# Optimization experiments

Measured on AMD Instinct MI355X. Metric: run time of the kernel, lower is better.

## Reference

```python
import jax, jax.numpy as jnp
import numpy as np
from jax import lax

B, CIN, H, W = 32, 256, 28, 28
COUT, KS, KEXP = 256, 3, 4
HIDDEN = int(CIN * 0.25)  # ratio hard-coded to 0.25 in the module


def setup_inputs() -> dict:
    key = jax.random.key(0)
    k1, k2, k3, k4 = jax.random.split(key, 4)
    x = jax.random.normal(k1, (B, CIN, H, W), dtype=jnp.float32)
    # SE (InvertedEx) params: fc1 (1x1 conv, no bias), fc2 (1x1 conv, bias)
    fc1_w = jax.random.normal(k2, (HIDDEN, CIN), dtype=jnp.float32) * np.float32(np.sqrt(2.0 / CIN))
    fc2_w = jax.random.normal(k3, (KEXP * COUT, HIDDEN), dtype=jnp.float32) * np.float32(np.sqrt(2.0 / HIDDEN))
    fc2_b = jnp.zeros((KEXP * COUT,), dtype=jnp.float32)
    # K expert conv kernels, he_std = sqrt(2) * (CIN*KS^2)^-0.5
    he_std = np.float32(np.sqrt(2.0) * (CIN * KS * KS) ** -0.5)
    weight = jax.random.normal(k4, (KEXP, COUT, CIN, KS, KS), dtype=jnp.float32) * he_std
    return {"x": x, "fc1_w": fc1_w, "fc2_w": fc2_w, "fc2_b": fc2_b, "weight": weight}


def reference(x, fc1_w, fc2_w, fc2_b, weight):
    # --- SE routing ---
    pooled = jnp.mean(x, axis=(2, 3))                        # [B, CIN]
    h = jax.nn.relu(pooled @ fc1_w.T)                        # [B, HIDDEN]
    y = (h @ fc2_w.T + fc2_b).reshape(B, KEXP, COUT)         # [B, K, COUT]
    prob = jax.nn.softmax(y / jnp.sqrt(jnp.float32(HIDDEN)), axis=1)  # softmax over K
    # --- aggregate per-sample kernels ---
    agg_w = jnp.einsum('bko,koihw->boihw', prob, weight)     # [B, COUT, CIN, KS, KS]
    # --- per-sample conv (batched implicit GEMM via vmap) ---
    def conv1(xi, wi):
        return lax.conv_general_dilated(
            xi[None], wi, window_strides=(1, 1), padding=((1, 1), (1, 1)),
            dimension_numbers=('NCHW', 'OIHW', 'NCHW'))[0]
    out = jax.vmap(conv1)(x, agg_w)                          # [B, COUT, H, W]
    return out
```

## Files before the change

### kernel.cpp

```cpp
#include <hip/hip_runtime.h>
#include <math.h>

#define B_    32
#define CIN_  256
#define HW_   784
#define H_    28
#define W_    28
#define COUT_ 256
#define KEXP_ 4
#define HID_  64

typedef short short8 __attribute__((ext_vector_type(8)));
typedef unsigned short ushort4v __attribute__((ext_vector_type(4)));
typedef unsigned short ushort8v __attribute__((ext_vector_type(8)));
typedef float floatx16 __attribute__((ext_vector_type(16)));

#define AS1 __attribute__((address_space(1)))
#define AS3 __attribute__((address_space(3)))
__device__ __forceinline__ void glds16(const void* g, void* l) {
    __builtin_amdgcn_global_load_lds((const AS1 unsigned int*)g,
                                     (AS3 unsigned int*)l, 16, 0, 0);
}
#define VMW(N) asm volatile("s_waitcnt vmcnt(" #N ")" ::: "memory")
#define SB()   __builtin_amdgcn_sched_barrier(0)

__device__ __forceinline__ unsigned short f2bf(float f) {
    union { float f; unsigned int u; } v; v.f = f;
    unsigned int r = (v.u + 0x7FFFu + ((v.u >> 16) & 1u)) >> 16;
    return (unsigned short)r;
}

__global__ __launch_bounds__(256) void xpose_pool_kernel(const float* __restrict__ x,
                                                         unsigned short* __restrict__ x_t,
                                                         float* __restrict__ partial,
                                                         float* __restrict__ zp) {
    __shared__ float tile[32][33];
    int bid = blockIdx.x;
    int b   = bid / 200;
    int rem = bid - b * 200;
    int icg = rem / 25;
    int pxt = rem % 25;
    int ic0 = icg * 32;
    int px0 = pxt * 32;
    int t = threadIdx.x;
    if (bid == 0 && t == 0) {
        float4 z; z.x = 0.f; z.y = 0.f; z.z = 0.f; z.w = 0.f;
        *(float4*)zp = z;
    }
    int c = t & 31, rr = t >> 5;
    #pragma unroll
    for (int r = 0; r < 4; ++r) {
        int icr = rr + r * 8;
        int px = px0 + c;
        float v = (px < HW_) ? x[((size_t)(b * CIN_ + ic0 + icr)) * HW_ + px] : 0.f;
        tile[icr][c] = v;
    }
    __syncthreads();
    #pragma unroll
    for (int r = 0; r < 4; ++r) {
        int pxr = rr + r * 8;
        int px = px0 + pxr;
        if (px < HW_)
            x_t[((size_t)b * HW_ + px) * CIN_ + ic0 + c] = f2bf(tile[c][pxr]);
    }
    if (t < 32) {
        float s = 0.f;
        #pragma unroll
        for (int cc = 0; cc < 32; ++cc) s += tile[t][cc];
        partial[((size_t)b * 25 + pxt) * CIN_ + ic0 + t] = s * (1.0f / HW_);
    }
}

__global__ __launch_bounds__(256) void pool_kernel(const float* __restrict__ x,
                                                   float* __restrict__ pooled) {
    int w = blockIdx.x * 4 + (threadIdx.x >> 6);
    int lane = threadIdx.x & 63;
    const float* p = x + (size_t)w * HW_;
    float s = 0.f;
    for (int i = lane; i < HW_; i += 64) s += p[i];
    for (int off = 32; off; off >>= 1) s += __shfl_down(s, off);
    if (lane == 0) pooled[w] = s * (1.0f / HW_);
}

__global__ __launch_bounds__(256) void se3_kernel(const float* __restrict__ partial,
                                                  const float* __restrict__ fc1_w,
                                                  const float* __restrict__ fc2_w,
                                                  const float* __restrict__ fc2_b,
                                                  float* __restrict__ prob) {
    __shared__ float pl[CIN_];
    __shared__ float h[HID_];
    __shared__ float wb[16640];
    int b = blockIdx.x, t = threadIdx.x;
    {
        float s = 0.f;
        for (int pt = 0; pt < 25; ++pt)
            s += partial[((size_t)b * 25 + pt) * CIN_ + t];
        pl[t] = s;
    }
    #pragma unroll
    for (int i = 0; i < 16; ++i) {
        int l = t + i * 256;
        float4 v = *(const float4*)(fc1_w + (size_t)l * 4);
        int r = l >> 6, cc = (l & 63) * 4;
        float* dst = &wb[r * 257 + cc];
        dst[0] = v.x; dst[1] = v.y; dst[2] = v.z; dst[3] = v.w;
    }
    __syncthreads();
    if (t < HID_) {
        float s = 0.f;
        const float* wr = &wb[t * 257];
        for (int c = 0; c < CIN_; ++c) s += pl[c] * wr[c];
        h[t] = fmaxf(s, 0.f);
    }
    float yk[KEXP_];
    for (int k = 0; k < KEXP_; ++k) {
        __syncthreads();
        #pragma unroll
        for (int i = 0; i < 16; ++i) {
            int l = t + i * 256;
            float4 v = *(const float4*)(fc2_w + (size_t)k * COUT_ * HID_ + (size_t)l * 4);
            int o = l >> 4, jj = (l & 15) * 4;
            float* dst = &wb[o * 65 + jj];
            dst[0] = v.x; dst[1] = v.y; dst[2] = v.z; dst[3] = v.w;
        }
        __syncthreads();
        float s = fc2_b[k * COUT_ + t];
        const float* wr = &wb[t * 65];
        #pragma unroll
        for (int j = 0; j < HID_; ++j) s += h[j] * wr[j];
        yk[k] = s * 0.125f;
    }
    float m = yk[0];
    for (int k = 1; k < KEXP_; ++k) m = fmaxf(m, yk[k]);
    float e[KEXP_], sum = 0.f;
    for (int k = 0; k < KEXP_; ++k) { e[k] = expf(yk[k] - m); sum += e[k]; }
    float inv = 1.0f / sum;
    for (int k = 0; k < KEXP_; ++k)
        prob[b * (KEXP_ * COUT_) + k * COUT_ + t] = e[k] * inv;
}

__global__ __launch_bounds__(256) void se2_kernel(const float* __restrict__ pooled,
                                                  const float* __restrict__ fc1_w,
                                                  const float* __restrict__ fc2_w,
                                                  const float* __restrict__ fc2_b,
                                                  float* __restrict__ prob) {
    __shared__ float pl[CIN_];
    __shared__ float h[HID_];
    __shared__ float wb[16640];
    int b = blockIdx.x, t = threadIdx.x;
    pl[t] = pooled[b * CIN_ + t];
    #pragma unroll
    for (int i = 0; i < 16; ++i) {
        int l = t + i * 256;
        float4 v = *(const float4*)(fc1_w + (size_t)l * 4);
        int r = l >> 6, cc = (l & 63) * 4;
        float* dst = &wb[r * 257 + cc];
        dst[0] = v.x; dst[1] = v.y; dst[2] = v.z; dst[3] = v.w;
    }
    __syncthreads();
    if (t < HID_) {
        float s = 0.f;
        const float* wr = &wb[t * 257];
        for (int c = 0; c < CIN_; ++c) s += pl[c] * wr[c];
        h[t] = fmaxf(s, 0.f);
    }
    float yk[KEXP_];
    for (int k = 0; k < KEXP_; ++k) {
        __syncthreads();
        #pragma unroll
        for (int i = 0; i < 16; ++i) {
            int l = t + i * 256;
            float4 v = *(const float4*)(fc2_w + (size_t)k * COUT_ * HID_ + (size_t)l * 4);
            int o = l >> 4, jj = (l & 15) * 4;
            float* dst = &wb[o * 65 + jj];
            dst[0] = v.x; dst[1] = v.y; dst[2] = v.z; dst[3] = v.w;
        }
        __syncthreads();
        float s = fc2_b[k * COUT_ + t];
        const float* wr = &wb[t * 65];
        #pragma unroll
        for (int j = 0; j < HID_; ++j) s += h[j] * wr[j];
        yk[k] = s * 0.125f;
    }
    float m = yk[0];
    for (int k = 1; k < KEXP_; ++k) m = fmaxf(m, yk[k]);
    float e[KEXP_], sum = 0.f;
    for (int k = 0; k < KEXP_; ++k) { e[k] = expf(yk[k] - m); sum += e[k]; }
    float inv = 1.0f / sum;
    for (int k = 0; k < KEXP_; ++k)
        prob[b * (KEXP_ * COUT_) + k * COUT_ + t] = e[k] * inv;
}

__global__ __launch_bounds__(256) void agg4_kernel(const float* __restrict__ weight,
                                                   const float* __restrict__ prob,
                                                   unsigned short* __restrict__ agg) {
    __shared__ float wlds[4][32][145];
    int gid = blockIdx.x;
    int og  = gid & 7;
    int icc = (gid >> 3) & 3;
    int kk  = (gid >> 5) & 3;
    int bh  = gid >> 7;
    int oc0 = og * 32;
    int ic0 = icc * 64 + kk * 16;
    int t = threadIdx.x;

    #pragma unroll
    for (int i = 0; i < 18; ++i) {
        int idx = t + i * 256;
        int k  = idx / 1152;
        int r  = idx - k * 1152;
        int oc = r / 36;
        int f4 = r - oc * 36;
        float4 v = *(const float4*)(weight + ((size_t)(k * COUT_ + oc0 + oc) * CIN_ + ic0) * 9 + f4 * 4);
        float* dst = &wlds[k][oc][f4 * 4];
        dst[0] = v.x; dst[1] = v.y; dst[2] = v.z; dst[3] = v.w;
    }

    int lane = t & 63, wv = t >> 6;
    int ml = lane & 31, kh = lane >> 5;

    float pbr[4][4];
    #pragma unroll
    for (int bi = 0; bi < 4; ++bi) {
        int b = bh * 16 + wv * 4 + bi;
        #pragma unroll
        for (int k = 0; k < 4; ++k)
            pbr[bi][k] = prob[(size_t)b * (KEXP_ * COUT_) + k * COUT_ + oc0 + ml];
    }
    __syncthreads();

    for (int rs = 0; rs < 9; ++rs) {
        float wreg[4][8];
        #pragma unroll
        for (int k = 0; k < 4; ++k)
            #pragma unroll
            for (int j = 0; j < 8; ++j)
                wreg[k][j] = wlds[k][ml][(kh * 8 + j) * 9 + rs];
        #pragma unroll
        for (int bi = 0; bi < 4; ++bi) {
            int b = bh * 16 + wv * 4 + bi;
            ushort8v pack;
            #pragma unroll
            for (int j = 0; j < 8; ++j) {
                float s = pbr[bi][0] * wreg[0][j] + pbr[bi][1] * wreg[1][j]
                        + pbr[bi][2] * wreg[2][j] + pbr[bi][3] * wreg[3][j];
                pack[j] = f2bf(s);
            }
            *(ushort8v*)(agg + (size_t)(b * 16 + icc * 4 + kk) * 36864
                             + (size_t)rs * 4096 + og * 512 + lane * 8) = pack;
        }
    }
}

__global__ __launch_bounds__(256, 2) void conv_mfma8_kernel(const unsigned short* __restrict__ x_t,
                                                            const unsigned short* __restrict__ agg,
                                                            const float* __restrict__ zp,
                                                            float* __restrict__ out) {
    __shared__ __align__(16) short Xs[2][6720];
    __shared__ __align__(16) short Alds[24576];

    int gid = blockIdx.x;
    int b      = gid & 31;
    int half   = (gid >> 5) & 1;
    int oc0    = half * 128;
    int rowblk = gid >> 6;
    int py0 = rowblk * 4;

    int t = threadIdx.x;
    int lane = t & 63, w = t >> 6;
    int ml = lane & 31, kh = lane >> 5;
    int og = half * 4 + w;
    int kh16 = kh << 4;

    floatx16 acc[4];
    #pragma unroll
    for (int j = 0; j < 4; ++j)
        #pragma unroll
        for (int r = 0; r < 16; ++r) acc[j][r] = 0.f;

    const unsigned short* xtb = x_t + (size_t)b * HW_ * CIN_;
    const unsigned short* ag  = agg + (size_t)b * 589824 + og * 512 + lane * 8;

    int off[3][6];
    #pragma unroll
    for (int dx = 0; dx < 3; ++dx)
        #pragma unroll
        for (int r = 0; r < 6; ++r) {
            int a = ml + dx + 35 * r;
            off[dx][r] = a * 64 + ((((a & 3) ^ ((a >> 2) & 1))) << 4);
        }

    auto stageXs = [&](int cc, int bb) {
        #pragma unroll
        for (int i = 0; i < 3; ++i) {
            int l = t + i * 256;
            int pos = l >> 2, gl = l & 3;
            int g8 = gl ^ (pos & 3) ^ ((pos >> 2) & 1);
            int row = pos / 35, col = pos - row * 35;
            int gy = py0 - 1 + row, gx = col - 1;
            const void* src = ((unsigned)gy < 28u && (unsigned)gx < 28u)
                ? (const void*)(xtb + ((size_t)(gy * W_ + gx)) * CIN_ + cc * 32 + g8 * 8)
                : (const void*)zp;
            glds16(src, &Xs[bb][(w * 64 + i * 256) * 8]);
        }
        if (w < 2) {
            int l = t + 768;
            int pos = l >> 2, gl = l & 3;
            int g8 = gl ^ (pos & 3) ^ ((pos >> 2) & 1);
            int row = pos / 35, col = pos - row * 35;
            int gy = py0 - 1 + row, gx = col - 1;
            const void* src = (l < 840 && (unsigned)gy < 28u && (unsigned)gx < 28u)
                ? (const void*)(xtb + ((size_t)(gy * W_ + gx)) * CIN_ + cc * 32 + g8 * 8)
                : (const void*)zp;
            if (l < 840)
                glds16(src, &Xs[bb][(w * 64 + 768) * 8]);
        }
    };

    auto dmaA = [&](int gg) {
        int c3  = gg / 6;
        int icc = c3 >> 1;
        int kk4 = (c3 & 1) * 2 + (gg % 6) / 3;
        int dx3 = gg % 3;
        const unsigned short* sp = ag + icc * 147456 + kk4 * 36864 + dx3 * 4096;
        short* d = &Alds[((w * 4 + (gg & 3)) * 3) * 512];
        glds16(sp,         d);
        glds16(sp + 12288, d + 512);
        glds16(sp + 24576, d + 1024);
    };

    stageXs(0, 0);  SB();
    dmaA(0);        SB();
    dmaA(1);        SB();
    dmaA(2);        SB();
    VMW(6);         SB();
    __builtin_amdgcn_s_barrier();

    short8 Areg[2][3];
    #pragma unroll
    for (int tap = 0; tap < 3; ++tap)
        Areg[0][tap] = *(const short8*)&Alds[((w * 4 + 0) * 3 + tap) * 512 + lane * 8];

    #pragma unroll
    for (int g = 0; g < 48; ++g) {
        const int c  = g / 6;
        const int s  = g % 6;
        const int kk = s / 3;
        const int dx = g % 3;

        if (g + 3 < 48)      { dmaA(g + 3);                  SB(); }
        if (s == 3 && c < 7) { stageXs(c + 1, (c + 1) & 1);  SB(); }

        if (g == 45)      { VMW(3); }
        else if (g == 46) { VMW(0); }
        else if (g < 45 && s >= 3 && c < 7) { VMW(9); }
        else if (g < 47)  { VMW(6); }
        SB();

        if (g < 47) {
            #pragma unroll
            for (int tap = 0; tap < 3; ++tap)
                Areg[(g + 1) & 1][tap] =
                    *(const short8*)&Alds[((w * 4 + ((g + 1) & 3)) * 3 + tap) * 512 + lane * 8];
        }

        const char* xbc = (const char*)&Xs[c & 1][0];
        const int kxor = (kk << 5) | kh16;
        #pragma unroll
        for (int r = 0; r < 6; ++r) {
            short8 Bf = *(const short8*)(xbc + (off[dx][r] ^ kxor));
            if (r <= 3)
                acc[r]     = __builtin_amdgcn_mfma_f32_32x32x16_bf16(Areg[g & 1][0], Bf, acc[r], 0, 0, 0);
            if (r >= 1 && r <= 4)
                acc[r - 1] = __builtin_amdgcn_mfma_f32_32x32x16_bf16(Areg[g & 1][1], Bf, acc[r - 1], 0, 0, 0);
            if (r >= 2)
                acc[r - 2] = __builtin_amdgcn_mfma_f32_32x32x16_bf16(Areg[g & 1][2], Bf, acc[r - 2], 0, 0, 0);
        }

        if (s == 5 && c < 7) {
            VMW(6);  SB();
            __builtin_amdgcn_s_barrier();
        }
    }

    if (ml < W_) {
        #pragma unroll
        for (int j = 0; j < 4; ++j) {
            float* op = out + ((size_t)(b * COUT_ + oc0 + w * 32)) * HW_ + (py0 + j) * W_ + ml;
            #pragma unroll
            for (int r = 0; r < 16; ++r) {
                int ocd = (r & 3) + 8 * (r >> 2) + 4 * kh;
                op[(size_t)ocd * HW_] = acc[j][r];
            }
        }
    }
}

__global__ __launch_bounds__(256) void conv_kernel(const float* __restrict__ x,
                                                   const float* __restrict__ weight,
                                                   const float* __restrict__ prob,
                                                   float* __restrict__ out) {
    __shared__ float xs[30 * 30];
    __shared__ float wagg[8][32][12];
    __shared__ float pl[KEXP_][8];

    int b  = blockIdx.x >> 5;
    int o0 = (blockIdx.x & 31) * 8;
    int t  = threadIdx.x;

    if (t < 32) {
        int k = t >> 3, oc = t & 7;
        pl[k][oc] = prob[b * (KEXP_ * COUT_) + k * COUT_ + o0 + oc];
    }
    int p0 = t;
    int pr[4], pc[4];
    bool pv[4];
    #pragma unroll
    for (int j = 0; j < 4; ++j) {
        int p = p0 + j * 256;
        pv[j] = p < HW_;
        pr[j] = p / W_;
        pc[j] = p % W_;
    }
    float acc[8][4];
    #pragma unroll
    for (int oc = 0; oc < 8; ++oc)
        #pragma unroll
        for (int j = 0; j < 4; ++j) acc[oc][j] = 0.f;

    int aoc = t >> 5, aii = t & 31;

    for (int ic0 = 0; ic0 < CIN_; ic0 += 32) {
        __syncthreads();
        {
            float w9[9];
            #pragma unroll
            for (int j = 0; j < 9; ++j) w9[j] = 0.f;
            int i = ic0 + aii;
            #pragma unroll
            for (int k = 0; k < KEXP_; ++k) {
                float pk = pl[k][aoc];
                const float* wp = weight + ((size_t)(k * COUT_ + o0 + aoc) * CIN_ + i) * 9;
                #pragma unroll
                for (int j = 0; j < 9; ++j) w9[j] += pk * wp[j];
            }
            #pragma unroll
            for (int j = 0; j < 9; ++j) wagg[aoc][aii][j] = w9[j];
        }
        for (int ii = 0; ii < 32; ++ii) {
            int i = ic0 + ii;
            __syncthreads();
            const float* xp = x + (size_t)(b * CIN_ + i) * HW_;
            for (int e = t; e < 900; e += 256) {
                int ry = e / 30, cx = e - ry * 30;
                int gy = ry - 1, gx = cx - 1;
                float v = 0.f;
                if ((unsigned)gy < 28u && (unsigned)gx < 28u) v = xp[gy * W_ + gx];
                xs[e] = v;
            }
            __syncthreads();
            float xv[4][9];
            #pragma unroll
            for (int j = 0; j < 4; ++j) {
                if (pv[j]) {
                    const float* xr = &xs[pr[j] * 30 + pc[j]];
                    xv[j][0] = xr[0];  xv[j][1] = xr[1];  xv[j][2] = xr[2];
                    xv[j][3] = xr[30]; xv[j][4] = xr[31]; xv[j][5] = xr[32];
                    xv[j][6] = xr[60]; xv[j][7] = xr[61]; xv[j][8] = xr[62];
                } else {
                    #pragma unroll
                    for (int q = 0; q < 9; ++q) xv[j][q] = 0.f;
                }
            }
            #pragma unroll
            for (int oc = 0; oc < 8; ++oc) {
                float4 wa = *(const float4*)&wagg[oc][ii][0];
                float4 wb2 = *(const float4*)&wagg[oc][ii][4];
                float  wc = wagg[oc][ii][8];
                #pragma unroll
                for (int j = 0; j < 4; ++j) {
                    acc[oc][j] += xv[j][0] * wa.x + xv[j][1] * wa.y + xv[j][2] * wa.z
                                + xv[j][3] * wa.w + xv[j][4] * wb2.x + xv[j][5] * wb2.y
                                + xv[j][6] * wb2.z + xv[j][7] * wb2.w + xv[j][8] * wc;
                }
            }
        }
    }
    #pragma unroll
    for (int oc = 0; oc < 8; ++oc) {
        float* op = out + (size_t)(b * COUT_ + o0 + oc) * HW_ + p0;
        #pragma unroll
        for (int j = 0; j < 4; ++j)
            if (pv[j]) op[j * 256] = acc[oc][j];
    }
}

extern "C" void kernel_launch(void* const* d_in, const int* in_sizes, int n_in,
                              void* d_out, int out_size, void* d_ws, size_t ws_size,
                              hipStream_t stream) {
    const float* x     = (const float*)d_in[0];
    const float* fc1_w = (const float*)d_in[1];
    const float* fc2_w = (const float*)d_in[2];
    const float* fc2_b = (const float*)d_in[3];
    const float* weight= (const float*)d_in[4];
    float* out = (float*)d_out;

    char* ws = (char*)d_ws;
    float* prob = (float*)(ws);
    unsigned short* x_t = (unsigned short*)(ws + 131072);
    unsigned short* agg = (unsigned short*)(ws + 12976128);
    float* partial = (float*)(ws + 12976128);
    float* zp   = (float*)(ws + 50724864);
    const size_t WS_NEED = 50724864 + 4096;

    if (ws_size >= WS_NEED) {
        xpose_pool_kernel<<<B_ * 8 * 25, 256, 0, stream>>>(x, x_t, partial, zp);
        se3_kernel<<<B_, 256, 0, stream>>>(partial, fc1_w, fc2_w, fc2_b, prob);
        agg4_kernel<<<256, 256, 0, stream>>>(weight, prob, agg);
        conv_mfma8_kernel<<<448, 256, 0, stream>>>(x_t, agg, zp, out);
    } else {
        float* pooled = (float*)(ws + 131072);
        pool_kernel<<<(B_ * CIN_) / 4, 256, 0, stream>>>(x, pooled);
        se2_kernel<<<B_, 256, 0, stream>>>(pooled, fc1_w, fc2_w, fc2_b, prob);
        conv_kernel<<<B_ * (COUT_ / 8), 256, 0, stream>>>(x, weight, prob, out);
    }
}
```

Measured before the change: 145.3 us.

## Enlarge conv tile to seven output rows per block with new LDS swizzle

The implicit-GEMM conv kernel now computes 7 output rows per block instead of 4, so the grid shrinks from 448 to 256 blocks and each A (aggregated weight) fragment is reused across more MFMAs. The X staging buffer grows for the taller halo and gets a new pair-based XOR swizzle. The A prefetch ring drops from 4 to 3 slots with a restructured per-chunk loop and a peeled final chunk. The goal is to cut weight reloads and per-block overhead. The cost is 7 accumulators per thread, so more register pressure, and 256 blocks may not fill all CUs on the GPU.

New measurement: 148.6 us. 1.02x slower.

```diff
diff --git a/kernel.cpp b/kernel.cpp
--- a/kernel.cpp
+++ b/kernel.cpp
@@ -252,140 +252,146 @@
     }
 }
 
-__global__ __launch_bounds__(256, 2) void conv_mfma8_kernel(const unsigned short* __restrict__ x_t,
+__global__ __launch_bounds__(256, 2) void conv_mfma9_kernel(const unsigned short* __restrict__ x_t,
                                                             const unsigned short* __restrict__ agg,
                                                             const float* __restrict__ zp,
                                                             float* __restrict__ out) {
-    __shared__ __align__(16) short Xs[2][6720];
-    __shared__ __align__(16) short Alds[24576];
+    __shared__ __align__(16) short Xs[2][10080];
+    __shared__ __align__(16) short Alds[18432];
 
     int gid = blockIdx.x;
     int b      = gid & 31;
     int half   = (gid >> 5) & 1;
     int oc0    = half * 128;
     int rowblk = gid >> 6;
-    int py0 = rowblk * 4;
+    int py0 = rowblk * 7;
 
     int t = threadIdx.x;
     int lane = t & 63, w = t >> 6;
     int ml = lane & 31, kh = lane >> 5;
     int og = half * 4 + w;
-    int kh16 = kh << 4;
-
-    floatx16 acc[4];
-    #pragma unroll
-    for (int j = 0; j < 4; ++j)
+
+    floatx16 acc[7];
+    #pragma unroll
+    for (int j = 0; j < 7; ++j)
         #pragma unroll
         for (int r = 0; r < 16; ++r) acc[j][r] = 0.f;
 
     const unsigned short* xtb = x_t + (size_t)b * HW_ * CIN_;
     const unsigned short* ag  = agg + (size_t)b * 589824 + og * 512 + lane * 8;
 
-    int off[3][6];
+    int off0[3][9];
     #pragma unroll
     for (int dx = 0; dx < 3; ++dx)
         #pragma unroll
-        for (int r = 0; r < 6; ++r) {
+        for (int r = 0; r < 9; ++r) {
             int a = ml + dx + 35 * r;
-            off[dx][r] = a * 64 + ((((a & 3) ^ ((a >> 2) & 1))) << 4);
+            int p = a >> 1;
+            int q0 = (((a & 1) << 2) | kh) ^ (p & 7);
+            off0[dx][r] = p * 128 + q0 * 16;
         }
 
     auto stageXs = [&](int cc, int bb) {
         #pragma unroll
-        for (int i = 0; i < 3; ++i) {
+        for (int i = 0; i < 5; ++i) {
             int l = t + i * 256;
-            int pos = l >> 2, gl = l & 3;
-            int g8 = gl ^ (pos & 3) ^ ((pos >> 2) & 1);
-            int row = pos / 35, col = pos - row * 35;
+            bool act = (l < 1260);
+            int pair = l >> 3, q = l & 7;
+            int v = q ^ (pair & 7);
+            int g8 = v & 3;
+            int a  = pair * 2 + (v >> 2);
+            int row = a / 35, col = a - row * 35;
             int gy = py0 - 1 + row, gx = col - 1;
-            const void* src = ((unsigned)gy < 28u && (unsigned)gx < 28u)
+            const void* src = (act && (unsigned)gy < 28u && (unsigned)gx < 28u)
                 ? (const void*)(xtb + ((size_t)(gy * W_ + gx)) * CIN_ + cc * 32 + g8 * 8)
                 : (const void*)zp;
-            glds16(src, &Xs[bb][(w * 64 + i * 256) * 8]);
-        }
-        if (w < 2) {
-            int l = t + 768;
-            int pos = l >> 2, gl = l & 3;
-            int g8 = gl ^ (pos & 3) ^ ((pos >> 2) & 1);
-            int row = pos / 35, col = pos - row * 35;
-            int gy = py0 - 1 + row, gx = col - 1;
-            const void* src = (l < 840 && (unsigned)gy < 28u && (unsigned)gx < 28u)
-                ? (const void*)(xtb + ((size_t)(gy * W_ + gx)) * CIN_ + cc * 32 + g8 * 8)
-                : (const void*)zp;
-            if (l < 840)
-                glds16(src, &Xs[bb][(w * 64 + 768) * 8]);
+            if (act)
+                glds16(src, &Xs[bb][(w * 64 + i * 256) * 8]);
         }
     };
 
-    auto dmaA = [&](int gg) {
-        int c3  = gg / 6;
-        int icc = c3 >> 1;
-        int kk4 = (c3 & 1) * 2 + (gg % 6) / 3;
-        int dx3 = gg % 3;
-        const unsigned short* sp = ag + icc * 147456 + kk4 * 36864 + dx3 * 4096;
-        short* d = &Alds[((w * 4 + (gg & 3)) * 3) * 512];
+    auto dmaA = [&](int cc, int kk2, int dx2, int slot) {
+        const unsigned short* sp = ag + (cc >> 1) * 147456
+                                      + ((cc & 1) * 2 + kk2) * 36864 + dx2 * 4096;
+        short* d = &Alds[(w * 9 + slot * 3) * 512];
         glds16(sp,         d);
         glds16(sp + 12288, d + 512);
         glds16(sp + 24576, d + 1024);
     };
 
-    stageXs(0, 0);  SB();
-    dmaA(0);        SB();
-    dmaA(1);        SB();
-    dmaA(2);        SB();
-    VMW(6);         SB();
+    stageXs(0, 0);     SB();
+    dmaA(0, 0, 0, 0);  SB();
+    dmaA(0, 0, 1, 1);  SB();
+    VMW(3);            SB();
     __builtin_amdgcn_s_barrier();
 
     short8 Areg[2][3];
     #pragma unroll
     for (int tap = 0; tap < 3; ++tap)
-        Areg[0][tap] = *(const short8*)&Alds[((w * 4 + 0) * 3 + tap) * 512 + lane * 8];
-
-    #pragma unroll
-    for (int g = 0; g < 48; ++g) {
-        const int c  = g / 6;
-        const int s  = g % 6;
-        const int kk = s / 3;
-        const int dx = g % 3;
-
-        if (g + 3 < 48)      { dmaA(g + 3);                  SB(); }
-        if (s == 3 && c < 7) { stageXs(c + 1, (c + 1) & 1);  SB(); }
-
-        if (g == 45)      { VMW(3); }
-        else if (g == 46) { VMW(0); }
-        else if (g < 45 && s >= 3 && c < 7) { VMW(9); }
-        else if (g < 47)  { VMW(6); }
-        SB();
-
-        if (g < 47) {
+        Areg[0][tap] = *(const short8*)&Alds[(w * 9 + tap) * 512 + lane * 8];
+
+    for (int c = 0; c < 7; ++c) {
+        const char* xb = (const char*)&Xs[0][0] + (c & 1) * 20160;
+        #pragma unroll
+        for (int s = 0; s < 6; ++s) {
+            if (s <= 3)      { dmaA(c,     (s + 2) / 3, (s + 2) % 3, (s + 2) % 3); SB(); }
+            else if (s == 4) { dmaA(c + 1, 0, 0, 0); SB(); }
+            else             { dmaA(c + 1, 0, 1, 1); SB(); }
+            if (s == 3) { stageXs(c + 1, (c + 1) & 1); SB(); }
+            if (s == 3 || s == 4) { VMW(8); } else { VMW(3); }
+            SB();
             #pragma unroll
             for (int tap = 0; tap < 3; ++tap)
-                Areg[(g + 1) & 1][tap] =
-                    *(const short8*)&Alds[((w * 4 + ((g + 1) & 3)) * 3 + tap) * 512 + lane * 8];
-        }
-
-        const char* xbc = (const char*)&Xs[c & 1][0];
-        const int kxor = (kk << 5) | kh16;
-        #pragma unroll
-        for (int r = 0; r < 6; ++r) {
-            short8 Bf = *(const short8*)(xbc + (off[dx][r] ^ kxor));
-            if (r <= 3)
-                acc[r]     = __builtin_amdgcn_mfma_f32_32x32x16_bf16(Areg[g & 1][0], Bf, acc[r], 0, 0, 0);
-            if (r >= 1 && r <= 4)
-                acc[r - 1] = __builtin_amdgcn_mfma_f32_32x32x16_bf16(Areg[g & 1][1], Bf, acc[r - 1], 0, 0, 0);
-            if (r >= 2)
-                acc[r - 2] = __builtin_amdgcn_mfma_f32_32x32x16_bf16(Areg[g & 1][2], Bf, acc[r - 2], 0, 0, 0);
-        }
-
-        if (s == 5 && c < 7) {
-            VMW(6);  SB();
-            __builtin_amdgcn_s_barrier();
+                Areg[(s + 1) & 1][tap] =
+                    *(const short8*)&Alds[(w * 9 + ((s + 1) % 3) * 3 + tap) * 512 + lane * 8];
+            const int kx = (s / 3) << 5;
+            const int dx = s % 3;
+            #pragma unroll
+            for (int r = 0; r < 9; ++r) {
+                short8 Bf = *(const short8*)(xb + (off0[dx][r] ^ kx));
+                if (r <= 6)
+                    acc[r]     = __builtin_amdgcn_mfma_f32_32x32x16_bf16(Areg[s & 1][0], Bf, acc[r], 0, 0, 0);
+                if (r >= 1 && r <= 7)
+                    acc[r - 1] = __builtin_amdgcn_mfma_f32_32x32x16_bf16(Areg[s & 1][1], Bf, acc[r - 1], 0, 0, 0);
+                if (r >= 2)
+                    acc[r - 2] = __builtin_amdgcn_mfma_f32_32x32x16_bf16(Areg[s & 1][2], Bf, acc[r - 2], 0, 0, 0);
+            }
+            if (s == 5) __builtin_amdgcn_s_barrier();
+        }
+    }
+
+    {
+        const char* xb = (const char*)&Xs[0][0] + 20160;
+        #pragma unroll
+        for (int s = 0; s < 6; ++s) {
+            if (s <= 3) { dmaA(7, (s + 2) / 3, (s + 2) % 3, (s + 2) % 3); SB(); }
+            if (s <= 3)      { VMW(3); }
+            else if (s == 4) { VMW(0); }
+            SB();
+            if (s < 5) {
+                #pragma unroll
+                for (int tap = 0; tap < 3; ++tap)
+                    Areg[(s + 1) & 1][tap] =
+                        *(const short8*)&Alds[(w * 9 + ((s + 1) % 3) * 3 + tap) * 512 + lane * 8];
+            }
+            const int kx = (s / 3) << 5;
+            const int dx = s % 3;
+            #pragma unroll
+            for (int r = 0; r < 9; ++r) {
+                short8 Bf = *(const short8*)(xb + (off0[dx][r] ^ kx));
+                if (r <= 6)
+                    acc[r]     = __builtin_amdgcn_mfma_f32_32x32x16_bf16(Areg[s & 1][0], Bf, acc[r], 0, 0, 0);
+                if (r >= 1 && r <= 7)
+                    acc[r - 1] = __builtin_amdgcn_mfma_f32_32x32x16_bf16(Areg[s & 1][1], Bf, acc[r - 1], 0, 0, 0);
+                if (r >= 2)
+                    acc[r - 2] = __builtin_amdgcn_mfma_f32_32x32x16_bf16(Areg[s & 1][2], Bf, acc[r - 2], 0, 0, 0);
+            }
         }
     }
 
     if (ml < W_) {
         #pragma unroll
-        for (int j = 0; j < 4; ++j) {
+        for (int j = 0; j < 7; ++j) {
             float* op = out + ((size_t)(b * COUT_ + oc0 + w * 32)) * HW_ + (py0 + j) * W_ + ml;
             #pragma unroll
             for (int r = 0; r < 16; ++r) {
@@ -517,7 +523,7 @@
         xpose_pool_kernel<<<B_ * 8 * 25, 256, 0, stream>>>(x, x_t, partial, zp);
         se3_kernel<<<B_, 256, 0, stream>>>(partial, fc1_w, fc2_w, fc2_b, prob);
         agg4_kernel<<<256, 256, 0, stream>>>(weight, prob, agg);
-        conv_mfma8_kernel<<<448, 256, 0, stream>>>(x_t, agg, zp, out);
+        conv_mfma9_kernel<<<256, 256, 0, stream>>>(x_t, agg, zp, out);
     } else {
         float* pooled = (float*)(ws + 131072);
         pool_kernel<<<(B_ * CIN_) / 4, 256, 0, stream>>>(x, pooled);
```
